# Kernel tuning notes

Measured on AMD Instinct MI355X. Metric: run time of the kernel, lower is better.

The kernel has to match this reference:

```python
import jax, jax.numpy as jnp
import numpy as np

B, T, D, H = 4, 2048, 768, 12
DH = D // H
SCALE = DH ** 0.5


def setup_inputs() -> dict:
    key = jax.random.key(0)
    k1, k2, k3, k4, k5, k6 = jax.random.split(key, 6)
    h = jax.random.normal(k1, (B, T, D), dtype=jnp.float32)
    key_padding_mask = jax.random.bernoulli(k2, 0.1, (B, T))
    s = 1.0 / np.sqrt(D)
    Wq = jax.random.normal(k3, (D, D), dtype=jnp.float32) * s
    Wk = jax.random.normal(k4, (D, D), dtype=jnp.float32) * s
    Wv = jax.random.normal(k5, (D, D), dtype=jnp.float32) * s
    Wo = jax.random.normal(k6, (D, D), dtype=jnp.float32) * s
    return {"h": h, "key_padding_mask": key_padding_mask,
            "Wq": Wq, "Wk": Wk, "Wv": Wv, "Wo": Wo}


def _split_heads(x):
    Bb, Tt, _ = x.shape
    return x.reshape(Bb, Tt, H, DH).transpose(0, 2, 1, 3)  # [B,H,T,Dh]


def reference(h, key_padding_mask, Wq, Wk, Wv, Wo):
    # torch nn.Linear (no bias): y = x @ W.T
    Q = _split_heads(h @ Wq.T)
    K = _split_heads(h @ Wk.T)
    V = _split_heads(h @ Wv.T)
    scores = jnp.einsum('bhqd,bhkd->bhqk', Q, K) / SCALE
    k_pad = key_padding_mask[:, None, None, :]  # mask padded keys
    q_pad = key_padding_mask[:, None, :, None]  # padded query rows
    scores = jnp.where(k_pad, jnp.float32(-1e9), scores)
    scores = jnp.where(q_pad, jnp.float32(0.0), scores)
    attn = jax.nn.softmax(scores, axis=-1)  # stable softmax (same math)
    attn = jnp.where(q_pad, jnp.float32(0.0), attn)
    out = jnp.einsum('bhqk,bhkd->bhqd', attn, V)  # [B,H,T,Dh]
    out = out.transpose(0, 2, 1, 3).reshape(B, T, D)
    return out @ Wo.T
```

## Files before the change

### kernel.cpp

```cpp
#include <hip/hip_runtime.h>
#include <stdint.h>

typedef __bf16 bf16x8 __attribute__((ext_vector_type(8)));
typedef float  f32x4  __attribute__((ext_vector_type(4)));
typedef float  f32x16 __attribute__((ext_vector_type(16)));
typedef unsigned short u16x4 __attribute__((ext_vector_type(4)));

#define MFMA16(a,b,c) __builtin_amdgcn_mfma_f32_16x16x32_bf16((a),(b),(c),0,0,0)
#define MFMA32(a,b,c) __builtin_amdgcn_mfma_f32_32x32x16_bf16((a),(b),(c),0,0,0)

constexpr int Bc  = 4;
constexpr int Tc  = 2048;
constexpr int Dc  = 768;
constexpr int Hc  = 12;
constexpr int NTOK = Bc * Tc;
constexpr int QKV_N = 3 * Dc;
constexpr int QK_LD = 2 * Dc;
constexpr int H4 = NTOK * Dc / 4;
constexpr int W4 = Dc * Dc / 4;

static __device__ __forceinline__ unsigned short f2bf(float f){
  unsigned u = __float_as_uint(f);
  u += 0x7fffu + ((u >> 16) & 1u);
  return (unsigned short)(u >> 16);
}

static __device__ __forceinline__ float exp2a(float x){
  float r; asm("v_exp_f32 %0, %1" : "=v"(r) : "v"(x)); return r;
}

static __device__ __forceinline__ float max3f(float a, float b, float c){
  float r; asm("v_max3_f32 %0, %1, %2, %3" : "=v"(r) : "v"(a), "v"(b), "v"(c)); return r;
}

static __device__ __forceinline__ unsigned cvtpk_bf16(float lo, float hi){
  unsigned r; asm("v_cvt_pk_bf16_f32 %0, %1, %2" : "=v"(r) : "v"(lo), "v"(hi)); return r;
}

static __device__ __forceinline__ void gload_lds16(const void* g, void* l){
  __builtin_amdgcn_global_load_lds((__attribute__((address_space(1))) void*)g,
                                   (__attribute__((address_space(3))) void*)l,
                                   16, 0, 0);
}

__global__ void prep(const float* __restrict__ h,  const float* __restrict__ Wq,
                     const float* __restrict__ Wk, const float* __restrict__ Wv,
                     const float* __restrict__ Wo,
                     unsigned short* __restrict__ hb,
                     unsigned short* __restrict__ Wqkv,
                     unsigned short* __restrict__ Wob, float qscale){
  const int idx = blockIdx.x * blockDim.x + threadIdx.x;
  const float* src; ushort4* dst; float sc = 1.0f; int r;
  if (idx < H4){
    src = h; dst = reinterpret_cast<ushort4*>(hb); r = idx;
  } else {
    const int j = idx - H4;
    const int y = j / W4;
    r = j - y * W4;
    if (y == 0){ src = Wq; sc = qscale; } else if (y == 1){ src = Wk; }
    else if (y == 2){ src = Wv; } else { src = Wo; }
    dst = (y == 3) ? reinterpret_cast<ushort4*>(Wob)
                   : reinterpret_cast<ushort4*>(Wqkv) + (size_t)y * W4;
  }
  float4 v = reinterpret_cast<const float4*>(src)[r];
  ushort4 o;
  o.x = f2bf(v.x * sc); o.y = f2bf(v.y * sc);
  o.z = f2bf(v.z * sc); o.w = f2bf(v.w * sc);
  dst[r] = o;
}

__global__ void expand_mask(const unsigned* __restrict__ raw, int* __restrict__ out, int n){
  __shared__ int sInt, sFlt;
  int t = threadIdx.x;
  if (t == 0){ sInt = 1; sFlt = 1; }
  __syncthreads();
  int okI = 1, okF = 1;
  for (int i = t; i < n/4; i += blockDim.x){
    unsigned u = raw[i];
    okI &= (u <= 1u);
    okF &= (u == 0u || u == 0x3f800000u);
  }
  if (!okI) atomicAnd(&sInt, 0);
  if (!okF) atomicAnd(&sFlt, 0);
  __syncthreads();
  if (sInt || sFlt){
    for (int i = t; i < n; i += blockDim.x) out[i] = (raw[i] != 0u);
  } else {
    const unsigned char* rb = (const unsigned char*)raw;
    for (int i = t; i < n; i += blockDim.x) out[i] = (rb[i] != 0);
  }
}

__global__ __launch_bounds__(256) void gemm_qkv(const unsigned short* __restrict__ A,
                                                const unsigned short* __restrict__ Bm,
                                                unsigned short* __restrict__ QKt,
                                                unsigned short* __restrict__ VtG,
                                                int M, int N, int K){
  __shared__ unsigned short As[128*64];
  __shared__ unsigned short Bs[128*64];
  const int t = threadIdx.x;
  const int w = t >> 6, l = t & 63;
  const int wr = w >> 1, wc = w & 1;
  const int lin = blockIdx.y * gridDim.x + blockIdx.x;
  const int swz = (lin & 7) * 144 + (lin >> 3);
  const int bxs = swz % 18, bys = swz / 18;
  const int br = bys * 128, bc = bxs * 128;

  f32x4 acc[4][4];
  const f32x4 fz = {0.f,0.f,0.f,0.f};
  #pragma unroll
  for (int m=0;m<4;m++)
    #pragma unroll
    for (int n=0;n<4;n++) acc[m][n] = fz;

  const int srow = l >> 3;
  const int scol = (l & 7) ^ srow;
  const int fr = l & 15;
  const int fu = l >> 4;

  for (int k0 = 0; k0 < K; k0 += 64){
    #pragma unroll
    for (int i = 0; i < 4; ++i){
      const int rb = w*32 + i*8;
      gload_lds16(A  + (size_t)(br + rb + srow)*K + k0 + scol*8, &As[rb*64]);
      gload_lds16(Bm + (size_t)(bc + rb + srow)*K + k0 + scol*8, &Bs[rb*64]);
    }
    __syncthreads();
    bf16x8 a[2][4], b[2][4];
    #pragma unroll
    for (int ks=0; ks<2; ks++){
      #pragma unroll
      for (int m=0;m<4;m++){
        const int row = wr*64 + m*16 + fr;
        a[ks][m] = *reinterpret_cast<const bf16x8*>(
            &As[row*64 + (((ks*4+fu) ^ (row&7))*8)]);
      }
      #pragma unroll
      for (int n=0;n<4;n++){
        const int row = wc*64 + n*16 + fr;
        b[ks][n] = *reinterpret_cast<const bf16x8*>(
            &Bs[row*64 + (((ks*4+fu) ^ (row&7))*8)]);
      }
    }
    #pragma unroll
    for (int ks=0; ks<2; ks++)
      #pragma unroll
      for (int m=0;m<4;m++)
        #pragma unroll
        for (int n=0;n<4;n++)
          acc[m][n] = MFMA16(a[ks][m], b[ks][n], acc[m][n]);
    __syncthreads();
  }

  const int orow0 = br + wr*64 + (l >> 4)*4;
  const int ocol0 = bc + wc*64 + (l & 15);
  if (bc >= QK_LD){
    #pragma unroll
    for (int m=0;m<4;m++){
      const int orow = orow0 + m*16;
      const int bb = orow >> 11, tok = orow & 2047;
      #pragma unroll
      for (int n=0;n<4;n++){
        const int cc = ocol0 + n*16 - QK_LD;
        const int hh = cc >> 6, dd = cc & 63;
        ushort4 o;
        o.x = f2bf(acc[m][n][0]); o.y = f2bf(acc[m][n][1]);
        o.z = f2bf(acc[m][n][2]); o.w = f2bf(acc[m][n][3]);
        *reinterpret_cast<ushort4*>(
            &VtG[((size_t)((bb*Hc + hh)*64 + dd))*Tc + tok]) = o;
      }
    }
  } else {
    #pragma unroll
    for (int m=0;m<4;m++)
      #pragma unroll
      for (int n=0;n<4;n++)
        #pragma unroll
        for (int r=0;r<4;r++)
          QKt[(size_t)(orow0 + m*16 + r) * QK_LD + (ocol0 + n*16)] =
              f2bf(acc[m][n][r]);
  }
}

__global__ __launch_bounds__(256) void gemm_bt64(const unsigned short* __restrict__ A,
                                                 const unsigned short* __restrict__ Bm,
                                                 float* __restrict__ C,
                                                 int M, int N, int K){
  __shared__ unsigned short As[64*32];
  __shared__ unsigned short Bs[128*32];
  const int t = threadIdx.x;
  const int w = t >> 6, l = t & 63;
  const int wr = w >> 1, wc = w & 1;
  const int lin = blockIdx.y * gridDim.x + blockIdx.x;
  const int swz = (lin & 7) * 96 + (lin >> 3);
  const int bxs = swz % 6, bys = swz / 6;
  const int br = bys * 64, bc = bxs * 128;

  f32x4 acc[2][4];
  const f32x4 fz = {0.f,0.f,0.f,0.f};
  #pragma unroll
  for (int m=0;m<2;m++)
    #pragma unroll
    for (int n=0;n<4;n++) acc[m][n] = fz;

  const int lrow = l >> 2;
  const int lk   = (l & 3) * 8;
  const int fr   = l & 15;
  const int fk   = (l >> 4) * 8;

  for (int k0 = 0; k0 < K; k0 += 32){
    gload_lds16(A + (size_t)(br + w*16 + lrow)*K + k0 + lk, &As[(w*16)*32]);
    #pragma unroll
    for (int it = 0; it < 2; ++it){
      const int rb = it*64 + w*16;
      gload_lds16(Bm + (size_t)(bc + rb + lrow)*K + k0 + lk, &Bs[rb*32]);
    }
    __syncthreads();
    bf16x8 a[2], b[4];
    #pragma unroll
    for (int m=0;m<2;m++)
      a[m] = *reinterpret_cast<const bf16x8*>(&As[(wr*32 + m*16 + fr)*32 + fk]);
    #pragma unroll
    for (int n=0;n<4;n++)
      b[n] = *reinterpret_cast<const bf16x8*>(&Bs[(wc*64 + n*16 + fr)*32 + fk]);
    #pragma unroll
    for (int m=0;m<2;m++)
      #pragma unroll
      for (int n=0;n<4;n++)
        acc[m][n] = MFMA16(a[m], b[n], acc[m][n]);
    __syncthreads();
  }

  const int orow0 = br + wr*32 + (l >> 4)*4;
  const int ocol0 = bc + wc*64 + (l & 15);
  #pragma unroll
  for (int m=0;m<2;m++)
    #pragma unroll
    for (int n=0;n<4;n++)
      #pragma unroll
      for (int r=0;r<4;r++)
        C[(size_t)(orow0 + m*16 + r) * N + (ocol0 + n*16)] = acc[m][n][r];
}

__global__ __launch_bounds__(256, 3) void attn(const unsigned short* __restrict__ QKt,
                                               const unsigned short* __restrict__ VtG,
                                               const int* __restrict__ mask,
                                               unsigned short* __restrict__ AO){
  __shared__ unsigned short Ks[2][64*64];
  __shared__ unsigned short Vs[2][64*64];
  __shared__ float Ms[2][64];

  const int t = threadIdx.x, w = t >> 6, l = t & 63;
  const int lin = blockIdx.y * gridDim.x + blockIdx.x;
  const int swz = (lin & 7) * 96 + (lin >> 3);
  const int qt  = swz & 15;
  const int bh  = swz >> 4;
  const int b  = bh / Hc, h = bh - b * Hc;
  const int lq = l & 31, hi = l >> 5;
  const int q0w = qt * 128 + w * 32;

  const size_t tokbase = (size_t)b * Tc;
  const unsigned short* Qp = QKt + (tokbase + q0w) * (size_t)QK_LD + h*64;
  const unsigned short* Kbase = QKt + tokbase * (size_t)QK_LD + h*64 + 768;
  const unsigned short* VtB = VtG + (size_t)(bh*64) * Tc;
  const int* bm = mask + b * Tc;

  bf16x8 qa[4];
  #pragma unroll
  for (int s=0; s<4; s++)
    qa[s] = *reinterpret_cast<const bf16x8*>(
        Qp + (size_t)lq*QK_LD + s*16 + hi*8);

  unsigned bits = 0;
  if (w == 0){
    #pragma unroll
    for (int cc = 0; cc < 32; ++cc)
      bits |= (unsigned)(bm[cc*64 + l] != 0) << cc;
  }

  f32x16 accO[2];
  #pragma unroll
  for (int dg=0; dg<2; dg++)
    #pragma unroll
    for (int r=0; r<16; r++) accO[dg][r] = 0.f;
  float mrow = -1e30f, lsum = 0.f;

  const int srow = l >> 3, scol = (l & 7) ^ (l >> 3);
  auto stage = [&](int c){
    const int key0 = c * 64, buf = c & 1;
    #pragma unroll
    for (int i=0; i<2; i++){
      const int rb = w*16 + i*8;
      gload_lds16(Kbase + (size_t)(key0 + rb + srow)*QK_LD + scol*8,
                  &Ks[buf][rb*64]);
    }
    #pragma unroll
    for (int i=0; i<2; i++){
      const int rb = (w*2 + i)*8;
      gload_lds16(VtB + (size_t)(rb + srow)*Tc + key0 + scol*8,
                  &Vs[buf][rb*64]);
    }
  };

  stage(0);
  if (w == 0) Ms[0][l] = (bits & 1u) ? -1e9f : 0.f;
  asm volatile("s_waitcnt vmcnt(0) lgkmcnt(0)" ::: "memory");
  __builtin_amdgcn_s_barrier();
  asm volatile("" ::: "memory");

  #pragma unroll 2
  for (int c = 0; c < 32; ++c){
    const int cb = c & 1;

    f32x16 S[2];
    __builtin_amdgcn_s_setprio(1);
    #pragma unroll
    for (int g=0; g<2; g++){
      union { f32x4 q[4]; f32x16 v; } mi;
      #pragma unroll
      for (int m=0; m<4; m++)
        mi.q[m] = *reinterpret_cast<const f32x4*>(&Ms[cb][g*32 + m*8 + hi*4]);
      S[g] = mi.v;
      #pragma unroll
      for (int s=0; s<4; s++){
        const int row = g*32 + lq;
        bf16x8 kf = *reinterpret_cast<const bf16x8*>(
            &Ks[cb][row*64 + (((2*s + hi) ^ (row&7))*8)]);
        S[g] = MFMA32(kf, qa[s], S[g]);
      }
    }
    __builtin_amdgcn_s_setprio(0);

    if (c + 1 < 32) stage(c + 1);

    unsigned pk[2][2][4];
    {
      float m0 = max3f(S[0][0],  S[0][1],  S[0][2]);
      float m1 = max3f(S[0][3],  S[0][4],  S[0][5]);
      float m2 = max3f(S[0][6],  S[0][7],  S[0][8]);
      float m3 = max3f(S[0][9],  S[0][10], S[0][11]);
      float m4 = max3f(S[0][12], S[0][13], S[0][14]);
      float m5 = max3f(S[0][15], S[1][0],  S[1][1]);
      float m6 = max3f(S[1][2],  S[1][3],  S[1][4]);
      float m7 = max3f(S[1][5],  S[1][6],  S[1][7]);
      float m8 = max3f(S[1][8],  S[1][9],  S[1][10]);
      float m9 = max3f(S[1][11], S[1][12], S[1][13]);
      float ma = fmaxf(S[1][14], S[1][15]);
      float cm = max3f(max3f(m0,m1,m2), max3f(m3,m4,m5),
                       max3f(max3f(m6,m7,m8), m9, ma));
      cm = fmaxf(cm, __shfl_xor(cm, 32));
      if (!__all(cm <= mrow + 8.0f)){
        const float nm = fmaxf(mrow, cm);
        const float sc = exp2a(mrow - nm);
        lsum *= sc;
        #pragma unroll
        for (int dg=0; dg<2; dg++)
          #pragma unroll
          for (int r=0; r<16; r++) accO[dg][r] *= sc;
        mrow = nm;
      }
      float ps = 0.f;
      #pragma unroll
      for (int g=0; g<2; g++){
        float p[16];
        #pragma unroll
        for (int r=0; r<16; r++) p[r] = exp2a(S[g][r] - mrow);
        float t0 = (p[0]+p[1]) + (p[2]+p[3]);
        float t1 = (p[4]+p[5]) + (p[6]+p[7]);
        float t2 = (p[8]+p[9]) + (p[10]+p[11]);
        float t3 = (p[12]+p[13]) + (p[14]+p[15]);
        ps += (t0+t1) + (t2+t3);
        #pragma unroll
        for (int ss=0; ss<2; ss++)
          #pragma unroll
          for (int j2=0; j2<4; j2++)
            pk[g][ss][j2] = cvtpk_bf16(p[ss*8 + 2*j2], p[ss*8 + 2*j2 + 1]);
      }
      ps += __shfl_xor(ps, 32);
      lsum += ps;
    }

    __builtin_amdgcn_s_setprio(1);
    #pragma unroll
    for (int g=0; g<2; g++){
      #pragma unroll
      for (int ss=0; ss<2; ss++){
        union { unsigned u[4]; bf16x8 v; } pb;
        pb.u[0] = pk[g][ss][0]; pb.u[1] = pk[g][ss][1];
        pb.u[2] = pk[g][ss][2]; pb.u[3] = pk[g][ss][3];
        const int u0 = 4*g + 2*ss;
        #pragma unroll
        for (int dg=0; dg<2; dg++){
          const int d = dg*32 + lq;
          union { u16x4 h[2]; bf16x8 v; } va;
          va.h[0] = *reinterpret_cast<const u16x4*>(
              &Vs[cb][d*64 + ((u0     ^ (d&7))*8) + hi*4]);
          va.h[1] = *reinterpret_cast<const u16x4*>(
              &Vs[cb][d*64 + (((u0+1) ^ (d&7))*8) + hi*4]);
          accO[dg] = MFMA32(va.v, pb.v, accO[dg]);
        }
      }
    }
    __builtin_amdgcn_s_setprio(0);

    if (w == 0 && c + 1 < 32)
      Ms[cb^1][l] = ((bits >> (c+1)) & 1u) ? -1e9f : 0.f;

    if (c < 31){
      asm volatile("s_waitcnt vmcnt(0) lgkmcnt(0)" ::: "memory");
      __builtin_amdgcn_s_barrier();
      asm volatile("" ::: "memory");
    }
  }

  {
    const int qrow = q0w + lq;
    const int qm = bm[qrow];
    const float inv = (qm || lsum <= 0.f) ? 0.f : 1.f / lsum;
    #pragma unroll
    for (int dg=0; dg<2; dg++)
      #pragma unroll
      for (int m=0; m<4; m++){
        ushort4 o;
        o.x = f2bf(accO[dg][4*m+0] * inv);
        o.y = f2bf(accO[dg][4*m+1] * inv);
        o.z = f2bf(accO[dg][4*m+2] * inv);
        o.w = f2bf(accO[dg][4*m+3] * inv);
        *reinterpret_cast<ushort4*>(
            &AO[(tokbase + qrow) * (size_t)Dc + h*64 + dg*32 + m*8 + hi*4]) = o;
      }
  }
}

extern "C" void kernel_launch(void* const* d_in, const int* in_sizes, int n_in,
                              void* d_out, int out_size, void* d_ws, size_t ws_size,
                              hipStream_t stream){
  const float* h    = (const float*)d_in[0];
  const unsigned* m = (const unsigned*)d_in[1];
  const float* Wq   = (const float*)d_in[2];
  const float* Wk   = (const float*)d_in[3];
  const float* Wv   = (const float*)d_in[4];
  const float* Wo   = (const float*)d_in[5];
  float* out        = (float*)d_out;

  unsigned short* hb   = (unsigned short*)d_ws;
  unsigned short* Wqkv = hb   + (size_t)NTOK * Dc;
  unsigned short* Wob  = Wqkv + (size_t)QKV_N * Dc;
  unsigned short* QKt  = Wob  + (size_t)Dc * Dc;
  unsigned short* VtG  = QKt  + (size_t)NTOK * QK_LD;
  unsigned short* AO   = VtG  + (size_t)NTOK * Dc;
  int* mexp            = (int*)(AO + (size_t)NTOK * Dc);

  const size_t need = ((size_t)NTOK*Dc + (size_t)QKV_N*Dc + (size_t)Dc*Dc +
                       (size_t)NTOK*QK_LD + (size_t)NTOK*Dc + (size_t)NTOK*Dc) * 2
                      + (size_t)NTOK*4;
  if (ws_size < need) return;

  prep<<<(H4 + 4*W4 + 255)/256, 256, 0, stream>>>(
      h, Wq, Wk, Wv, Wo, hb, Wqkv, Wob, 0.125f*1.44269504f);
  expand_mask<<<1, 256, 0, stream>>>(m, mexp, NTOK);

  gemm_qkv<<<dim3(QKV_N/128, NTOK/128), 256, 0, stream>>>(
      hb, Wqkv, QKt, VtG, NTOK, QKV_N, Dc);

  attn<<<dim3(16, Bc*Hc), 256, 0, stream>>>(QKt, VtG, mexp, AO);

  gemm_bt64<<<dim3(Dc/128, NTOK/64), 256, 0, stream>>>(
      AO, Wob, out, NTOK, Dc, Dc);
}
```

Measured before the change: 170.2 us.

## Triple-buffer K/V tiles and overlap next QK MFMA with current softmax

Moves the attention kernel from double to triple-buffered LDS for K, V and mask tiles, prefetching two chunks ahead. It also software-pipelines the loop so the QK^T MFMAs for chunk c+1 are issued between the max/rescale and exp phases of chunk c, using ping-pong score registers. The aim is to hide global-load latency and overlap the matrix units with the softmax ALU work. In exchange it uses more LDS and more registers for the second score set, which may lower occupancy under the 3-blocks-per-CU launch bound.

```diff
diff --git a/kernel.cpp b/kernel.cpp
--- a/kernel.cpp
+++ b/kernel.cpp
@@ -246,9 +246,9 @@
                                                const unsigned short* __restrict__ VtG,
                                                const int* __restrict__ mask,
                                                unsigned short* __restrict__ AO){
-  __shared__ unsigned short Ks[2][64*64];
-  __shared__ unsigned short Vs[2][64*64];
-  __shared__ float Ms[2][64];
+  __shared__ unsigned short Ks[3][64*64];
+  __shared__ unsigned short Vs[3][64*64];
+  __shared__ float Ms[3][64];
 
   const int t = threadIdx.x, w = t >> 6, l = t & 63;
   const int lin = blockIdx.y * gridDim.x + blockIdx.x;
@@ -287,7 +287,7 @@
 
   const int srow = l >> 3, scol = (l & 7) ^ (l >> 3);
   auto stage = [&](int c){
-    const int key0 = c * 64, buf = c & 1;
+    const int key0 = c * 64, buf = c % 3;
     #pragma unroll
     for (int i=0; i<2; i++){
       const int rb = w*16 + i*8;
@@ -302,50 +302,53 @@
     }
   };
 
-  stage(0);
-  if (w == 0) Ms[0][l] = (bits & 1u) ? -1e9f : 0.f;
+  auto qk = [&](int c, f32x16 (&S)[2]){
+    const int buf = c % 3;
+    #pragma unroll
+    for (int g=0; g<2; g++){
+      union { f32x4 q[4]; f32x16 v; } mi;
+      #pragma unroll
+      for (int m=0; m<4; m++)
+        mi.q[m] = *reinterpret_cast<const f32x4*>(&Ms[buf][g*32 + m*8 + hi*4]);
+      S[g] = mi.v;
+      #pragma unroll
+      for (int s=0; s<4; s++){
+        const int row = g*32 + lq;
+        bf16x8 kf = *reinterpret_cast<const bf16x8*>(
+            &Ks[buf][row*64 + (((2*s + hi) ^ (row&7))*8)]);
+        S[g] = MFMA32(kf, qa[s], S[g]);
+      }
+    }
+  };
+
+  f32x16 SA[2], SB[2];
+
+  stage(0); stage(1);
+  if (w == 0){
+    Ms[0][l] = (bits & 1u) ? -1e9f : 0.f;
+    Ms[1][l] = (bits & 2u) ? -1e9f : 0.f;
+  }
   asm volatile("s_waitcnt vmcnt(0) lgkmcnt(0)" ::: "memory");
   __builtin_amdgcn_s_barrier();
   asm volatile("" ::: "memory");
-
-  #pragma unroll 2
-  for (int c = 0; c < 32; ++c){
-    const int cb = c & 1;
-
-    f32x16 S[2];
-    __builtin_amdgcn_s_setprio(1);
-    #pragma unroll
-    for (int g=0; g<2; g++){
-      union { f32x4 q[4]; f32x16 v; } mi;
-      #pragma unroll
-      for (int m=0; m<4; m++)
-        mi.q[m] = *reinterpret_cast<const f32x4*>(&Ms[cb][g*32 + m*8 + hi*4]);
-      S[g] = mi.v;
-      #pragma unroll
-      for (int s=0; s<4; s++){
-        const int row = g*32 + lq;
-        bf16x8 kf = *reinterpret_cast<const bf16x8*>(
-            &Ks[cb][row*64 + (((2*s + hi) ^ (row&7))*8)]);
-        S[g] = MFMA32(kf, qa[s], S[g]);
-      }
-    }
-    __builtin_amdgcn_s_setprio(0);
-
-    if (c + 1 < 32) stage(c + 1);
-
-    unsigned pk[2][2][4];
+  qk(0, SA);
+
+  auto body = [&](int c, f32x16 (&Scur)[2], f32x16 (&Snxt)[2]){
+    const int cb = c % 3;
+    if (c + 2 < 32) stage(c + 2);
+
     {
-      float m0 = max3f(S[0][0],  S[0][1],  S[0][2]);
-      float m1 = max3f(S[0][3],  S[0][4],  S[0][5]);
-      float m2 = max3f(S[0][6],  S[0][7],  S[0][8]);
-      float m3 = max3f(S[0][9],  S[0][10], S[0][11]);
-      float m4 = max3f(S[0][12], S[0][13], S[0][14]);
-      float m5 = max3f(S[0][15], S[1][0],  S[1][1]);
-      float m6 = max3f(S[1][2],  S[1][3],  S[1][4]);
-      float m7 = max3f(S[1][5],  S[1][6],  S[1][7]);
-      float m8 = max3f(S[1][8],  S[1][9],  S[1][10]);
-      float m9 = max3f(S[1][11], S[1][12], S[1][13]);
-      float ma = fmaxf(S[1][14], S[1][15]);
+      float m0 = max3f(Scur[0][0],  Scur[0][1],  Scur[0][2]);
+      float m1 = max3f(Scur[0][3],  Scur[0][4],  Scur[0][5]);
+      float m2 = max3f(Scur[0][6],  Scur[0][7],  Scur[0][8]);
+      float m3 = max3f(Scur[0][9],  Scur[0][10], Scur[0][11]);
+      float m4 = max3f(Scur[0][12], Scur[0][13], Scur[0][14]);
+      float m5 = max3f(Scur[0][15], Scur[1][0],  Scur[1][1]);
+      float m6 = max3f(Scur[1][2],  Scur[1][3],  Scur[1][4]);
+      float m7 = max3f(Scur[1][5],  Scur[1][6],  Scur[1][7]);
+      float m8 = max3f(Scur[1][8],  Scur[1][9],  Scur[1][10]);
+      float m9 = max3f(Scur[1][11], Scur[1][12], Scur[1][13]);
+      float ma = fmaxf(Scur[1][14], Scur[1][15]);
       float cm = max3f(max3f(m0,m1,m2), max3f(m3,m4,m5),
                        max3f(max3f(m6,m7,m8), m9, ma));
       cm = fmaxf(cm, __shfl_xor(cm, 32));
@@ -359,12 +362,18 @@
           for (int r=0; r<16; r++) accO[dg][r] *= sc;
         mrow = nm;
       }
+    }
+
+    if (c + 1 < 32) qk(c + 1, Snxt);
+
+    unsigned pk[2][2][4];
+    {
       float ps = 0.f;
       #pragma unroll
       for (int g=0; g<2; g++){
         float p[16];
         #pragma unroll
-        for (int r=0; r<16; r++) p[r] = exp2a(S[g][r] - mrow);
+        for (int r=0; r<16; r++) p[r] = exp2a(Scur[g][r] - mrow);
         float t0 = (p[0]+p[1]) + (p[2]+p[3]);
         float t1 = (p[4]+p[5]) + (p[6]+p[7]);
         float t2 = (p[8]+p[9]) + (p[10]+p[11]);
@@ -403,14 +412,20 @@
     }
     __builtin_amdgcn_s_setprio(0);
 
-    if (w == 0 && c + 1 < 32)
-      Ms[cb^1][l] = ((bits >> (c+1)) & 1u) ? -1e9f : 0.f;
+    if (w == 0 && c + 2 < 32)
+      Ms[(c+2)%3][l] = ((bits >> (c+2)) & 1u) ? -1e9f : 0.f;
 
     if (c < 31){
       asm volatile("s_waitcnt vmcnt(0) lgkmcnt(0)" ::: "memory");
       __builtin_amdgcn_s_barrier();
       asm volatile("" ::: "memory");
     }
+  };
+
+  #pragma unroll 1
+  for (int cc = 0; cc < 16; ++cc){
+    body(2*cc,     SA, SB);
+    body(2*cc + 1, SB, SA);
   }
 
   {
```

New measurement: 183.0 us. 7.5% more time.

## Fold mask expansion into prep kernel and deepen output GEMM K-tile with LDS swizzle

Applied to the files above, without the earlier changes.

Mask expansion moves into an extra last block of the prep kernel, which removes one kernel launch. The output projection GEMM now steps 64 along K per iteration instead of 32, which halves the number of barrier-synchronised iterations. Its LDS tiles use an XOR swizzle on 16-byte chunks to avoid bank conflicts on the fragment reads. The cost is a larger LDS footprint per block and more registers for the doubled fragments.

```diff
diff --git a/kernel.cpp b/kernel.cpp
--- a/kernel.cpp
+++ b/kernel.cpp
@@ -48,7 +48,30 @@
                      const float* __restrict__ Wo,
                      unsigned short* __restrict__ hb,
                      unsigned short* __restrict__ Wqkv,
-                     unsigned short* __restrict__ Wob, float qscale){
+                     unsigned short* __restrict__ Wob, float qscale,
+                     const unsigned* __restrict__ raw, int* __restrict__ mout){
+  if (blockIdx.x == gridDim.x - 1){
+    __shared__ int sInt, sFlt;
+    const int t = threadIdx.x, n = NTOK;
+    if (t == 0){ sInt = 1; sFlt = 1; }
+    __syncthreads();
+    int okI = 1, okF = 1;
+    for (int i = t; i < n/4; i += blockDim.x){
+      unsigned u = raw[i];
+      okI &= (u <= 1u);
+      okF &= (u == 0u || u == 0x3f800000u);
+    }
+    if (!okI) atomicAnd(&sInt, 0);
+    if (!okF) atomicAnd(&sFlt, 0);
+    __syncthreads();
+    if (sInt || sFlt){
+      for (int i = t; i < n; i += blockDim.x) mout[i] = (raw[i] != 0u);
+    } else {
+      const unsigned char* rb = (const unsigned char*)raw;
+      for (int i = t; i < n; i += blockDim.x) mout[i] = (rb[i] != 0);
+    }
+    return;
+  }
   const int idx = blockIdx.x * blockDim.x + threadIdx.x;
   const float* src; ushort4* dst; float sc = 1.0f; int r;
   if (idx < H4){
@@ -67,28 +90,6 @@
   o.x = f2bf(v.x * sc); o.y = f2bf(v.y * sc);
   o.z = f2bf(v.z * sc); o.w = f2bf(v.w * sc);
   dst[r] = o;
-}
-
-__global__ void expand_mask(const unsigned* __restrict__ raw, int* __restrict__ out, int n){
-  __shared__ int sInt, sFlt;
-  int t = threadIdx.x;
-  if (t == 0){ sInt = 1; sFlt = 1; }
-  __syncthreads();
-  int okI = 1, okF = 1;
-  for (int i = t; i < n/4; i += blockDim.x){
-    unsigned u = raw[i];
-    okI &= (u <= 1u);
-    okF &= (u == 0u || u == 0x3f800000u);
-  }
-  if (!okI) atomicAnd(&sInt, 0);
-  if (!okF) atomicAnd(&sFlt, 0);
-  __syncthreads();
-  if (sInt || sFlt){
-    for (int i = t; i < n; i += blockDim.x) out[i] = (raw[i] != 0u);
-  } else {
-    const unsigned char* rb = (const unsigned char*)raw;
-    for (int i = t; i < n; i += blockDim.x) out[i] = (rb[i] != 0);
-  }
 }
 
 __global__ __launch_bounds__(256) void gemm_qkv(const unsigned short* __restrict__ A,
@@ -186,8 +187,8 @@
                                                  const unsigned short* __restrict__ Bm,
                                                  float* __restrict__ C,
                                                  int M, int N, int K){
-  __shared__ unsigned short As[64*32];
-  __shared__ unsigned short Bs[128*32];
+  __shared__ unsigned short As[64*64];
+  __shared__ unsigned short Bs[128*64];
   const int t = threadIdx.x;
   const int w = t >> 6, l = t & 63;
   const int wr = w >> 1, wc = w & 1;
@@ -203,31 +204,46 @@
     #pragma unroll
     for (int n=0;n<4;n++) acc[m][n] = fz;
 
-  const int lrow = l >> 2;
-  const int lk   = (l & 3) * 8;
-  const int fr   = l & 15;
-  const int fk   = (l >> 4) * 8;
-
-  for (int k0 = 0; k0 < K; k0 += 32){
-    gload_lds16(A + (size_t)(br + w*16 + lrow)*K + k0 + lk, &As[(w*16)*32]);
-    #pragma unroll
-    for (int it = 0; it < 2; ++it){
-      const int rb = it*64 + w*16;
-      gload_lds16(Bm + (size_t)(bc + rb + lrow)*K + k0 + lk, &Bs[rb*32]);
-    }
-    __syncthreads();
-    bf16x8 a[2], b[4];
-    #pragma unroll
-    for (int m=0;m<2;m++)
-      a[m] = *reinterpret_cast<const bf16x8*>(&As[(wr*32 + m*16 + fr)*32 + fk]);
-    #pragma unroll
-    for (int n=0;n<4;n++)
-      b[n] = *reinterpret_cast<const bf16x8*>(&Bs[(wc*64 + n*16 + fr)*32 + fk]);
-    #pragma unroll
-    for (int m=0;m<2;m++)
-      #pragma unroll
-      for (int n=0;n<4;n++)
-        acc[m][n] = MFMA16(a[m], b[n], acc[m][n]);
+  const int srow = l >> 3;
+  const int scol = (l & 7) ^ srow;
+  const int fr = l & 15;
+  const int fu = l >> 4;
+
+  for (int k0 = 0; k0 < K; k0 += 64){
+    #pragma unroll
+    for (int i = 0; i < 2; ++i){
+      const int rb = w*16 + i*8;
+      gload_lds16(A + (size_t)(br + rb + srow)*K + k0 + scol*8, &As[rb*64]);
+    }
+    #pragma unroll
+    for (int i = 0; i < 4; ++i){
+      const int rb = w*32 + i*8;
+      gload_lds16(Bm + (size_t)(bc + rb + srow)*K + k0 + scol*8, &Bs[rb*64]);
+    }
+    __syncthreads();
+    bf16x8 a[2][2], b[2][4];
+    #pragma unroll
+    for (int ks=0; ks<2; ks++){
+      #pragma unroll
+      for (int m=0;m<2;m++){
+        const int row = wr*32 + m*16 + fr;
+        a[ks][m] = *reinterpret_cast<const bf16x8*>(
+            &As[row*64 + (((ks*4+fu) ^ (row&7))*8)]);
+      }
+      #pragma unroll
+      for (int n=0;n<4;n++){
+        const int row = wc*64 + n*16 + fr;
+        b[ks][n] = *reinterpret_cast<const bf16x8*>(
+            &Bs[row*64 + (((ks*4+fu) ^ (row&7))*8)]);
+      }
+    }
+    #pragma unroll
+    for (int ks=0; ks<2; ks++)
+      #pragma unroll
+      for (int m=0;m<2;m++)
+        #pragma unroll
+        for (int n=0;n<4;n++)
+          acc[m][n] = MFMA16(a[ks][m], b[ks][n], acc[m][n]);
     __syncthreads();
   }
 
@@ -456,9 +472,8 @@
                       + (size_t)NTOK*4;
   if (ws_size < need) return;
 
-  prep<<<(H4 + 4*W4 + 255)/256, 256, 0, stream>>>(
-      h, Wq, Wk, Wv, Wo, hb, Wqkv, Wob, 0.125f*1.44269504f);
-  expand_mask<<<1, 256, 0, stream>>>(m, mexp, NTOK);
+  prep<<<(H4 + 4*W4)/256 + 1, 256, 0, stream>>>(
+      h, Wq, Wk, Wv, Wo, hb, Wqkv, Wob, 0.125f*1.44269504f, m, mexp);
 
   gemm_qkv<<<dim3(QKV_N/128, NTOK/128), 256, 0, stream>>>(
       hb, Wqkv, QKt, VtG, NTOK, QKV_N, Dc);
```

New measurement: 162.4 us. -4.6%, faster.
